# Optimization experiments

Measured on AMD Instinct MI355X. Metric: run time of the kernel, lower is better.

Reference implementation:

```python
import jax, jax.numpy as jnp
import numpy as np

EMBED_DIM = 64
N_EMBED = 1024
BATCH, H, W = 16, 64, 64


def setup_inputs() -> dict:
    key = jax.random.key(0)
    k1, k2 = jax.random.split(key)
    inputs = jax.random.normal(k1, (BATCH, H, W, EMBED_DIM), dtype=jnp.float32)
    # codebook as in Quantize.build: RandomNormal(stddev=1.0), shape (embed_dim, n_embed)
    cluster_mean = jax.random.normal(k2, (EMBED_DIM, N_EMBED), dtype=jnp.float32)
    return {"inputs": inputs, "cluster_mean": cluster_mean}


def reference(inputs, cluster_mean):
    # inputs: [B,H,W,D]; cluster_mean: [D,K]
    D = cluster_mean.shape[0]
    samples = inputs.reshape(-1, D)  # [N,D]
    dist = (
        jnp.sum(samples * samples, axis=1, keepdims=True)
        - 2.0 * (samples @ cluster_mean)
        + jnp.sum(cluster_mean * cluster_mean, axis=0, keepdims=True)
    )
    cluster_index = jnp.argmin(dist, axis=1).reshape(inputs.shape[:-1])  # [B,H,W]
    quantize = cluster_mean.T[cluster_index]  # gather -> [B,H,W,D]
    q_loss = jnp.mean((quantize - jax.lax.stop_gradient(inputs)) ** 2)
    e_loss = jnp.mean((jax.lax.stop_gradient(quantize) - inputs) ** 2)
    loss = q_loss + 0.25 * e_loss
    # straight-through estimator
    outputs = inputs + jax.lax.stop_gradient(quantize - inputs)
    return outputs, cluster_index, loss
```

## Files before the change

### kernel.cpp

```cpp
#include <hip/hip_runtime.h>
#include <stdint.h>

#define NS 65536
#define D 64
#define K 1024
#define NEL 4194304
#define MARGIN 0.05f

typedef short bf16x8 __attribute__((ext_vector_type(8)));
typedef float f32x4 __attribute__((ext_vector_type(4)));

static __device__ __forceinline__ unsigned short bf16_rne(float x) {
    union { float f; uint32_t u; } v; v.f = x;
    uint32_t r = v.u + 0x7FFFu + ((v.u >> 16) & 1u);
    return (unsigned short)(r >> 16);
}
static __device__ __forceinline__ float bf16f(unsigned short h) {
    union { uint32_t u; float f; } v; v.u = ((uint32_t)h) << 16;
    return v.f;
}

__global__ __launch_bounds__(256) void vq_prep(
    const float* __restrict__ cm,
    unsigned short* __restrict__ mhi,
    unsigned short* __restrict__ mlo,
    float* __restrict__ cnorm,
    double* __restrict__ acc)
{
    const int tx = threadIdx.x;
    const int kl = tx & 63, dq = tx >> 6;
    const int k = blockIdx.x * 64 + kl;
    if (blockIdx.x == 0 && tx == 0) *acc = 0.0;

    unsigned short h[16], lo[16];
    float p = 0.f;
#pragma unroll
    for (int j = 0; j < 16; ++j) {
        float v = cm[(dq*16 + j) * K + k];
        unsigned short hb = bf16_rne(v);
        h[j] = hb;
        lo[j] = bf16_rne(v - bf16f(hb));
        p = fmaf(v, v, p);
    }
    bf16x8 v0, v1, w0, w1;
#pragma unroll
    for (int j = 0; j < 8; ++j) {
        v0[j] = (short)h[j];  v1[j] = (short)h[8+j];
        w0[j] = (short)lo[j]; w1[j] = (short)lo[8+j];
    }
    *(bf16x8*)(mhi + (size_t)k*D + dq*16)     = v0;
    *(bf16x8*)(mhi + (size_t)k*D + dq*16 + 8) = v1;
    *(bf16x8*)(mlo + (size_t)k*D + dq*16)     = w0;
    *(bf16x8*)(mlo + (size_t)k*D + dq*16 + 8) = w1;

    __shared__ float pn[4][64];
    pn[dq][kl] = p;
    __syncthreads();
    if (tx < 64)
        cnorm[blockIdx.x*64 + tx] = (pn[0][tx]+pn[1][tx]) + (pn[2][tx]+pn[3][tx]);
}

__global__ __launch_bounds__(256, 4) void vq_main(
    const float* __restrict__ xin,
    const float* __restrict__ cm,
    const unsigned short* __restrict__ mhi,
    const unsigned short* __restrict__ mlo,
    const float* __restrict__ cnorm,
    float* __restrict__ outq,
    float* __restrict__ outidx,
    double* __restrict__ acc_g)
{
    __shared__ char smemA[18432];
    __shared__ unsigned short btile[2][2048];
    __shared__ float cn_lds[1024];
    __shared__ int   widx[64];

    unsigned short* xh = (unsigned short*)smemA;
    unsigned short* xl = (unsigned short*)(smemA + 9216);
    float* mb1 = (float*)smemA;
    float* mb2 = (float*)(smemA + 4096);
    int*   mi1 = (int*)(smemA + 8192);
    int*   mi2 = (int*)(smemA + 12288);
    float* red = (float*)smemA;

    const int tx = threadIdx.x;
    const int S0 = blockIdx.x * 64;
    const int w = tx >> 6, l = tx & 63;
    const int quad = l >> 4, col = l & 15;

    const unsigned short* stage_src = (w & 2) ? mlo : mhi;
    const int qh = ((w & 1) << 2) + quad;
    const unsigned short* stage_gp0 = stage_src + (size_t)col*D + qh*8;

    __builtin_amdgcn_global_load_lds(stage_gp0, &btile[0][w*512], 16, 0, 0);

    {
        const int s = tx >> 2, d0 = (tx & 3) * 16;
        const float* gp = xin + (size_t)(S0 + s) * D + d0;
        bf16x8 hv0, hv1, lv0, lv1;
#pragma unroll
        for (int j = 0; j < 8; ++j) {
            float va = gp[j], vb = gp[8 + j];
            unsigned short ha = bf16_rne(va), hb = bf16_rne(vb);
            hv0[j] = (short)ha; hv1[j] = (short)hb;
            lv0[j] = (short)bf16_rne(va - bf16f(ha));
            lv1[j] = (short)bf16_rne(vb - bf16f(hb));
        }
        *(bf16x8*)(xh + s*72 + d0)     = hv0;
        *(bf16x8*)(xh + s*72 + d0 + 8) = hv1;
        *(bf16x8*)(xl + s*72 + d0)     = lv0;
        *(bf16x8*)(xl + s*72 + d0 + 8) = lv1;
#pragma unroll
        for (int q = 0; q < 4; ++q) cn_lds[q*256 + tx] = cnorm[q*256 + tx];
    }
    __syncthreads();

    const int srow = w*16 + col;
    bf16x8 ahi0 = *(const bf16x8*)(xh + srow*72 + quad*8);
    bf16x8 ahi1 = *(const bf16x8*)(xh + srow*72 + 32 + quad*8);
    bf16x8 alo0 = *(const bf16x8*)(xl + srow*72 + quad*8);
    bf16x8 alo1 = *(const bf16x8*)(xl + srow*72 + 32 + quad*8);

    float b1[4], b2[4]; int i1[4], i2[4];
#pragma unroll
    for (int r = 0; r < 4; ++r) { b1[r]=3.4e38f; b2[r]=3.4e38f; i1[r]=0; i2[r]=0; }

    for (int t = 0; t < 64; ++t) {
        if (t > 0) __syncthreads();
        if (t < 63) {
            const unsigned short* gp = stage_gp0 + (size_t)(t+1)*16*D;
            __builtin_amdgcn_global_load_lds(gp, &btile[(t+1)&1][w*512], 16, 0, 0);
        }
        const unsigned short* bt = btile[t&1];
        bf16x8 bh0 = *(const bf16x8*)(bt + l*8);
        bf16x8 bh1 = *(const bf16x8*)(bt + 512  + l*8);
        bf16x8 bl0 = *(const bf16x8*)(bt + 1024 + l*8);
        bf16x8 bl1 = *(const bf16x8*)(bt + 1536 + l*8);
        f32x4 z = {0.f, 0.f, 0.f, 0.f};
        f32x4 hh = __builtin_amdgcn_mfma_f32_16x16x32_bf16(ahi0, bh0, z, 0,0,0);
        hh       = __builtin_amdgcn_mfma_f32_16x16x32_bf16(ahi1, bh1, hh, 0,0,0);
        f32x4 hl = __builtin_amdgcn_mfma_f32_16x16x32_bf16(ahi0, bl0, z, 0,0,0);
        hl       = __builtin_amdgcn_mfma_f32_16x16x32_bf16(ahi1, bl1, hl, 0,0,0);
        f32x4 lh = __builtin_amdgcn_mfma_f32_16x16x32_bf16(alo0, bh0, z, 0,0,0);
        lh       = __builtin_amdgcn_mfma_f32_16x16x32_bf16(alo1, bh1, lh, 0,0,0);
        const int kcode = t*16 + col;
        const float cn = cn_lds[kcode];
#pragma unroll
        for (int r = 0; r < 4; ++r) {
            float dot = (hh[r] + hl[r]) + lh[r];
            float d = fmaf(-2.f, dot, cn);
            bool c1 = d < b1[r];
            bool c2 = d < b2[r];
            b2[r] = c1 ? b1[r] : (c2 ? d : b2[r]);
            i2[r] = c1 ? i1[r] : (c2 ? kcode : i2[r]);
            b1[r] = c1 ? d : b1[r];
            i1[r] = c1 ? kcode : i1[r];
        }
        __syncthreads();
    }

#pragma unroll
    for (int r = 0; r < 4; ++r) {
        mb1[tx*4 + r] = b1[r];
        mb2[tx*4 + r] = b2[r];
        mi1[tx*4 + r] = i1[r];
        mi2[tx*4 + r] = i2[r];
    }
    __syncthreads();

    if (tx < 64) {
        const int mw = tx >> 4, mq = (tx >> 2) & 3, mr = tx & 3;
        float B1 = 3.4e38f, B2 = 3.4e38f; int I1 = 0, I2 = 0;
#pragma unroll
        for (int c = 0; c < 16; ++c) {
            const int e = (mw*64 + mq*16 + c)*4 + mr;
            float v1 = mb1[e]; int j1 = mi1[e];
            float v2 = mb2[e]; int j2 = mi2[e];
            if (v1 < B1)      { B2 = B1; I2 = I1; B1 = v1; I1 = j1; }
            else if (v1 < B2) { B2 = v1; I2 = j1; }
            if (v2 < B1)      { B2 = B1; I2 = I1; B1 = v2; I1 = j2; }
            else if (v2 < B2) { B2 = v2; I2 = j2; }
        }
        int winner = I1;
        if (B2 - B1 < MARGIN) {
            const float* xp = xin + (size_t)(S0 + tx) * D;
            float a0=0,a1=0,a2=0,a3=0, e0=0,e1=0,e2=0,e3=0;
            for (int dd = 0; dd < D; dd += 4) {
                float x0 = xp[dd], x1 = xp[dd+1], x2 = xp[dd+2], x3 = xp[dd+3];
                a0 = fmaf(x0, cm[(dd+0)*K + I1], a0);
                a1 = fmaf(x1, cm[(dd+1)*K + I1], a1);
                a2 = fmaf(x2, cm[(dd+2)*K + I1], a2);
                a3 = fmaf(x3, cm[(dd+3)*K + I1], a3);
                e0 = fmaf(x0, cm[(dd+0)*K + I2], e0);
                e1 = fmaf(x1, cm[(dd+1)*K + I2], e1);
                e2 = fmaf(x2, cm[(dd+2)*K + I2], e2);
                e3 = fmaf(x3, cm[(dd+3)*K + I2], e3);
            }
            float d1 = fmaf(-2.f, (a0+a1)+(a2+a3), cn_lds[I1]);
            float d2 = fmaf(-2.f, (e0+e1)+(e2+e3), cn_lds[I2]);
            if (d2 < d1 || (d2 == d1 && I2 < I1)) winner = I2;
        }
        widx[tx] = winner;
    }
    __syncthreads();

    const int sl = tx >> 2, d0 = (tx & 3) * 16;
    const int gs = S0 + sl;
    const int wi = widx[sl];
    const unsigned short* mh = mhi + (size_t)wi*D + d0;
    const unsigned short* ml = mlo + (size_t)wi*D + d0;
    bf16x8 h0 = *(const bf16x8*)(mh);
    bf16x8 h1 = *(const bf16x8*)(mh + 8);
    bf16x8 l0 = *(const bf16x8*)(ml);
    bf16x8 l1 = *(const bf16x8*)(ml + 8);
    const float* xr = xin + (size_t)gs*D + d0;
    float* oq = outq + (size_t)gs*D + d0;
    float psum = 0.f;
#pragma unroll
    for (int g = 0; g < 4; ++g) {
        float4 xv = *(const float4*)(xr + 4*g);
        float q0 = bf16f((unsigned short)(g < 2 ? h0[4*g+0] : h1[4*g-8+0])) +
                   bf16f((unsigned short)(g < 2 ? l0[4*g+0] : l1[4*g-8+0]));
        float q1 = bf16f((unsigned short)(g < 2 ? h0[4*g+1] : h1[4*g-8+1])) +
                   bf16f((unsigned short)(g < 2 ? l0[4*g+1] : l1[4*g-8+1]));
        float q2 = bf16f((unsigned short)(g < 2 ? h0[4*g+2] : h1[4*g-8+2])) +
                   bf16f((unsigned short)(g < 2 ? l0[4*g+2] : l1[4*g-8+2]));
        float q3 = bf16f((unsigned short)(g < 2 ? h0[4*g+3] : h1[4*g-8+3])) +
                   bf16f((unsigned short)(g < 2 ? l0[4*g+3] : l1[4*g-8+3]));
        float dx = q0 - xv.x, dy = q1 - xv.y, dz = q2 - xv.z, dw = q3 - xv.w;
        float4 o;
        o.x = xv.x + dx; o.y = xv.y + dy; o.z = xv.z + dz; o.w = xv.w + dw;
        *(float4*)(oq + 4*g) = o;
        psum = fmaf(dx, dx, psum);
        psum = fmaf(dy, dy, psum);
        psum = fmaf(dz, dz, psum);
        psum = fmaf(dw, dw, psum);
    }

    if (tx < 64)
        outidx[S0 + tx] = (float)widx[tx];

    red[tx] = psum;
    __syncthreads();
    for (int st = 128; st > 0; st >>= 1) {
        if (tx < st) red[tx] += red[tx + st];
        __syncthreads();
    }
    if (tx == 0) atomicAdd(acc_g, (double)red[0]);
}

__global__ void vq_finalize(const double* __restrict__ acc,
                            float* __restrict__ loss_out)
{
    float m = (float)(*acc / (double)NEL);
    *loss_out = m + 0.25f * m;
}

extern "C" void kernel_launch(void* const* d_in, const int* in_sizes, int n_in,
                              void* d_out, int out_size, void* d_ws, size_t ws_size,
                              hipStream_t stream) {
    const float* xin = (const float*)d_in[0];
    const float* cm  = (const float*)d_in[1];

    float* out     = (float*)d_out;
    float* outq    = out;
    float* outidx  = out + NEL;
    float* outloss = out + NEL + NS;

    unsigned short* mhi = (unsigned short*)d_ws;
    unsigned short* mlo = mhi + (size_t)K * D;
    float*  cnorm = (float*)((char*)d_ws + 262144);
    double* acc   = (double*)((char*)d_ws + 266240);

    vq_prep<<<16, 256, 0, stream>>>(cm, mhi, mlo, cnorm, acc);
    vq_main<<<1024, 256, 0, stream>>>(xin, cm, mhi, mlo, cnorm, outq, outidx, acc);
    vq_finalize<<<1, 1, 0, stream>>>(acc, outloss);
}
```

Before: 133.6 us.

## Load codebook fragments directly to registers, drop LDS staging and barriers

The main loop no longer stages codebook tiles through LDS with global_load_lds and two barriers per step. Each lane now prefetches its bf16 hi/lo fragments straight from global (L2-resident) into registers one step ahead. The three partial MFMA accumulators are merged into one chain, and the top-2 update uses fmed3/fmin. The prep kernel is spread over more blocks, and the merge scratch is padded to avoid bank conflicts. The aim is to remove barrier stalls and LDS traffic, at the cost of redundant global loads across waves and a serial MFMA dependency chain.

```diff
diff --git a/kernel.cpp b/kernel.cpp
--- a/kernel.cpp
+++ b/kernel.cpp
@@ -8,6 +8,7 @@
 #define MARGIN 0.05f
 
 typedef short bf16x8 __attribute__((ext_vector_type(8)));
+typedef short s16x4 __attribute__((ext_vector_type(4)));
 typedef float f32x4 __attribute__((ext_vector_type(4)));
 
 static __device__ __forceinline__ unsigned short bf16_rne(float x) {
@@ -28,36 +29,33 @@
     double* __restrict__ acc)
 {
     const int tx = threadIdx.x;
-    const int kl = tx & 63, dq = tx >> 6;
-    const int k = blockIdx.x * 64 + kl;
+    const int kl = tx & 15;
+    const int dg = tx >> 4;
+    const int k = blockIdx.x * 16 + kl;
     if (blockIdx.x == 0 && tx == 0) *acc = 0.0;
 
-    unsigned short h[16], lo[16];
     float p = 0.f;
-#pragma unroll
-    for (int j = 0; j < 16; ++j) {
-        float v = cm[(dq*16 + j) * K + k];
+    s16x4 hv, lv;
+#pragma unroll
+    for (int j = 0; j < 4; ++j) {
+        float v = cm[(dg * 4 + j) * K + k];
         unsigned short hb = bf16_rne(v);
-        h[j] = hb;
-        lo[j] = bf16_rne(v - bf16f(hb));
+        hv[j] = (short)hb;
+        lv[j] = (short)bf16_rne(v - bf16f(hb));
         p = fmaf(v, v, p);
     }
-    bf16x8 v0, v1, w0, w1;
-#pragma unroll
-    for (int j = 0; j < 8; ++j) {
-        v0[j] = (short)h[j];  v1[j] = (short)h[8+j];
-        w0[j] = (short)lo[j]; w1[j] = (short)lo[8+j];
-    }
-    *(bf16x8*)(mhi + (size_t)k*D + dq*16)     = v0;
-    *(bf16x8*)(mhi + (size_t)k*D + dq*16 + 8) = v1;
-    *(bf16x8*)(mlo + (size_t)k*D + dq*16)     = w0;
-    *(bf16x8*)(mlo + (size_t)k*D + dq*16 + 8) = w1;
-
-    __shared__ float pn[4][64];
-    pn[dq][kl] = p;
-    __syncthreads();
-    if (tx < 64)
-        cnorm[blockIdx.x*64 + tx] = (pn[0][tx]+pn[1][tx]) + (pn[2][tx]+pn[3][tx]);
+    *(s16x4*)(mhi + (size_t)k * D + dg * 4) = hv;
+    *(s16x4*)(mlo + (size_t)k * D + dg * 4) = lv;
+
+    __shared__ float pn[16][17];
+    pn[kl][dg] = p;
+    __syncthreads();
+    if (tx < 16) {
+        float s = 0.f;
+#pragma unroll
+        for (int g = 0; g < 16; ++g) s += pn[tx][g];
+        cnorm[blockIdx.x * 16 + tx] = s;
+    }
 }
 
 __global__ __launch_bounds__(256, 4) void vq_main(
@@ -71,16 +69,15 @@
     double* __restrict__ acc_g)
 {
     __shared__ char smemA[18432];
-    __shared__ unsigned short btile[2][2048];
     __shared__ float cn_lds[1024];
     __shared__ int   widx[64];
 
     unsigned short* xh = (unsigned short*)smemA;
     unsigned short* xl = (unsigned short*)(smemA + 9216);
     float* mb1 = (float*)smemA;
-    float* mb2 = (float*)(smemA + 4096);
-    int*   mi1 = (int*)(smemA + 8192);
-    int*   mi2 = (int*)(smemA + 12288);
+    float* mb2 = (float*)(smemA + 4352);
+    int*   mi1 = (int*)(smemA + 8704);
+    int*   mi2 = (int*)(smemA + 13056);
     float* red = (float*)smemA;
 
     const int tx = threadIdx.x;
@@ -88,11 +85,12 @@
     const int w = tx >> 6, l = tx & 63;
     const int quad = l >> 4, col = l & 15;
 
-    const unsigned short* stage_src = (w & 2) ? mlo : mhi;
-    const int qh = ((w & 1) << 2) + quad;
-    const unsigned short* stage_gp0 = stage_src + (size_t)col*D + qh*8;
-
-    __builtin_amdgcn_global_load_lds(stage_gp0, &btile[0][w*512], 16, 0, 0);
+    const unsigned short* ph = mhi + (size_t)col * D + quad * 8;
+    const unsigned short* pl = mlo + (size_t)col * D + quad * 8;
+    bf16x8 nh0 = *(const bf16x8*)(ph);
+    bf16x8 nh1 = *(const bf16x8*)(ph + 32);
+    bf16x8 nl0 = *(const bf16x8*)(pl);
+    bf16x8 nl1 = *(const bf16x8*)(pl + 32);
 
     {
         const int s = tx >> 2, d0 = (tx & 3) * 16;
@@ -106,65 +104,63 @@
             lv0[j] = (short)bf16_rne(va - bf16f(ha));
             lv1[j] = (short)bf16_rne(vb - bf16f(hb));
         }
-        *(bf16x8*)(xh + s*72 + d0)     = hv0;
-        *(bf16x8*)(xh + s*72 + d0 + 8) = hv1;
-        *(bf16x8*)(xl + s*72 + d0)     = lv0;
-        *(bf16x8*)(xl + s*72 + d0 + 8) = lv1;
-#pragma unroll
-        for (int q = 0; q < 4; ++q) cn_lds[q*256 + tx] = cnorm[q*256 + tx];
-    }
-    __syncthreads();
-
-    const int srow = w*16 + col;
-    bf16x8 ahi0 = *(const bf16x8*)(xh + srow*72 + quad*8);
-    bf16x8 ahi1 = *(const bf16x8*)(xh + srow*72 + 32 + quad*8);
-    bf16x8 alo0 = *(const bf16x8*)(xl + srow*72 + quad*8);
-    bf16x8 alo1 = *(const bf16x8*)(xl + srow*72 + 32 + quad*8);
+        *(bf16x8*)(xh + s * 72 + d0)     = hv0;
+        *(bf16x8*)(xh + s * 72 + d0 + 8) = hv1;
+        *(bf16x8*)(xl + s * 72 + d0)     = lv0;
+        *(bf16x8*)(xl + s * 72 + d0 + 8) = lv1;
+#pragma unroll
+        for (int q = 0; q < 4; ++q) cn_lds[q * 256 + tx] = cnorm[q * 256 + tx];
+    }
+    __syncthreads();
+
+    const int srow = w * 16 + col;
+    bf16x8 ahi0 = *(const bf16x8*)(xh + srow * 72 + quad * 8);
+    bf16x8 ahi1 = *(const bf16x8*)(xh + srow * 72 + 32 + quad * 8);
+    bf16x8 alo0 = *(const bf16x8*)(xl + srow * 72 + quad * 8);
+    bf16x8 alo1 = *(const bf16x8*)(xl + srow * 72 + 32 + quad * 8);
 
     float b1[4], b2[4]; int i1[4], i2[4];
 #pragma unroll
-    for (int r = 0; r < 4; ++r) { b1[r]=3.4e38f; b2[r]=3.4e38f; i1[r]=0; i2[r]=0; }
-
+    for (int r = 0; r < 4; ++r) { b1[r] = 3.4e38f; b2[r] = 3.4e38f; i1[r] = 0; i2[r] = 0; }
+
+#pragma unroll 2
     for (int t = 0; t < 64; ++t) {
-        if (t > 0) __syncthreads();
+        bf16x8 bh0 = nh0, bh1 = nh1, bl0 = nl0, bl1 = nl1;
+        ph += 16 * D; pl += 16 * D;
         if (t < 63) {
-            const unsigned short* gp = stage_gp0 + (size_t)(t+1)*16*D;
-            __builtin_amdgcn_global_load_lds(gp, &btile[(t+1)&1][w*512], 16, 0, 0);
-        }
-        const unsigned short* bt = btile[t&1];
-        bf16x8 bh0 = *(const bf16x8*)(bt + l*8);
-        bf16x8 bh1 = *(const bf16x8*)(bt + 512  + l*8);
-        bf16x8 bl0 = *(const bf16x8*)(bt + 1024 + l*8);
-        bf16x8 bl1 = *(const bf16x8*)(bt + 1536 + l*8);
-        f32x4 z = {0.f, 0.f, 0.f, 0.f};
-        f32x4 hh = __builtin_amdgcn_mfma_f32_16x16x32_bf16(ahi0, bh0, z, 0,0,0);
-        hh       = __builtin_amdgcn_mfma_f32_16x16x32_bf16(ahi1, bh1, hh, 0,0,0);
-        f32x4 hl = __builtin_amdgcn_mfma_f32_16x16x32_bf16(ahi0, bl0, z, 0,0,0);
-        hl       = __builtin_amdgcn_mfma_f32_16x16x32_bf16(ahi1, bl1, hl, 0,0,0);
-        f32x4 lh = __builtin_amdgcn_mfma_f32_16x16x32_bf16(alo0, bh0, z, 0,0,0);
-        lh       = __builtin_amdgcn_mfma_f32_16x16x32_bf16(alo1, bh1, lh, 0,0,0);
-        const int kcode = t*16 + col;
+            nh0 = *(const bf16x8*)(ph);
+            nh1 = *(const bf16x8*)(ph + 32);
+            nl0 = *(const bf16x8*)(pl);
+            nl1 = *(const bf16x8*)(pl + 32);
+        }
+        const int kcode = t * 16 + col;
         const float cn = cn_lds[kcode];
+        f32x4 acc = {0.f, 0.f, 0.f, 0.f};
+        acc = __builtin_amdgcn_mfma_f32_16x16x32_bf16(ahi0, bh0, acc, 0, 0, 0);
+        acc = __builtin_amdgcn_mfma_f32_16x16x32_bf16(ahi1, bh1, acc, 0, 0, 0);
+        acc = __builtin_amdgcn_mfma_f32_16x16x32_bf16(ahi0, bl0, acc, 0, 0, 0);
+        acc = __builtin_amdgcn_mfma_f32_16x16x32_bf16(ahi1, bl1, acc, 0, 0, 0);
+        acc = __builtin_amdgcn_mfma_f32_16x16x32_bf16(alo0, bh0, acc, 0, 0, 0);
+        acc = __builtin_amdgcn_mfma_f32_16x16x32_bf16(alo1, bh1, acc, 0, 0, 0);
 #pragma unroll
         for (int r = 0; r < 4; ++r) {
-            float dot = (hh[r] + hl[r]) + lh[r];
-            float d = fmaf(-2.f, dot, cn);
-            bool c1 = d < b1[r];
-            bool c2 = d < b2[r];
-            b2[r] = c1 ? b1[r] : (c2 ? d : b2[r]);
+            float dv = fmaf(-2.f, acc[r], cn);
+            bool c1 = dv < b1[r];
+            bool c2 = dv < b2[r];
+            b2[r] = __builtin_amdgcn_fmed3f(b1[r], dv, b2[r]);
+            b1[r] = fminf(b1[r], dv);
             i2[r] = c1 ? i1[r] : (c2 ? kcode : i2[r]);
-            b1[r] = c1 ? d : b1[r];
             i1[r] = c1 ? kcode : i1[r];
         }
-        __syncthreads();
-    }
-
+    }
+
+    const int sk = 4 * (tx + (tx >> 4));
 #pragma unroll
     for (int r = 0; r < 4; ++r) {
-        mb1[tx*4 + r] = b1[r];
-        mb2[tx*4 + r] = b2[r];
-        mi1[tx*4 + r] = i1[r];
-        mi2[tx*4 + r] = i2[r];
+        mb1[sk + r] = b1[r];
+        mb2[sk + r] = b2[r];
+        mi1[sk + r] = i1[r];
+        mi2[sk + r] = i2[r];
     }
     __syncthreads();
 
@@ -173,7 +169,8 @@
         float B1 = 3.4e38f, B2 = 3.4e38f; int I1 = 0, I2 = 0;
 #pragma unroll
         for (int c = 0; c < 16; ++c) {
-            const int e = (mw*64 + mq*16 + c)*4 + mr;
+            const int tw = mw * 64 + mq * 16 + c;
+            const int e = 4 * (tw + (tw >> 4)) + mr;
             float v1 = mb1[e]; int j1 = mi1[e];
             float v2 = mb2[e]; int j2 = mi2[e];
             if (v1 < B1)      { B2 = B1; I2 = I1; B1 = v1; I1 = j1; }
@@ -184,20 +181,20 @@
         int winner = I1;
         if (B2 - B1 < MARGIN) {
             const float* xp = xin + (size_t)(S0 + tx) * D;
-            float a0=0,a1=0,a2=0,a3=0, e0=0,e1=0,e2=0,e3=0;
+            float a0 = 0, a1 = 0, a2 = 0, a3 = 0, e0 = 0, e1 = 0, e2 = 0, e3 = 0;
             for (int dd = 0; dd < D; dd += 4) {
-                float x0 = xp[dd], x1 = xp[dd+1], x2 = xp[dd+2], x3 = xp[dd+3];
-                a0 = fmaf(x0, cm[(dd+0)*K + I1], a0);
-                a1 = fmaf(x1, cm[(dd+1)*K + I1], a1);
-                a2 = fmaf(x2, cm[(dd+2)*K + I1], a2);
-                a3 = fmaf(x3, cm[(dd+3)*K + I1], a3);
-                e0 = fmaf(x0, cm[(dd+0)*K + I2], e0);
-                e1 = fmaf(x1, cm[(dd+1)*K + I2], e1);
-                e2 = fmaf(x2, cm[(dd+2)*K + I2], e2);
-                e3 = fmaf(x3, cm[(dd+3)*K + I2], e3);
+                float x0 = xp[dd], x1 = xp[dd + 1], x2 = xp[dd + 2], x3 = xp[dd + 3];
+                a0 = fmaf(x0, cm[(dd + 0) * K + I1], a0);
+                a1 = fmaf(x1, cm[(dd + 1) * K + I1], a1);
+                a2 = fmaf(x2, cm[(dd + 2) * K + I1], a2);
+                a3 = fmaf(x3, cm[(dd + 3) * K + I1], a3);
+                e0 = fmaf(x0, cm[(dd + 0) * K + I2], e0);
+                e1 = fmaf(x1, cm[(dd + 1) * K + I2], e1);
+                e2 = fmaf(x2, cm[(dd + 2) * K + I2], e2);
+                e3 = fmaf(x3, cm[(dd + 3) * K + I2], e3);
             }
-            float d1 = fmaf(-2.f, (a0+a1)+(a2+a3), cn_lds[I1]);
-            float d2 = fmaf(-2.f, (e0+e1)+(e2+e3), cn_lds[I2]);
+            float d1 = fmaf(-2.f, (a0 + a1) + (a2 + a3), cn_lds[I1]);
+            float d2 = fmaf(-2.f, (e0 + e1) + (e2 + e3), cn_lds[I2]);
             if (d2 < d1 || (d2 == d1 && I2 < I1)) winner = I2;
         }
         widx[tx] = winner;
@@ -207,30 +204,30 @@
     const int sl = tx >> 2, d0 = (tx & 3) * 16;
     const int gs = S0 + sl;
     const int wi = widx[sl];
-    const unsigned short* mh = mhi + (size_t)wi*D + d0;
-    const unsigned short* ml = mlo + (size_t)wi*D + d0;
+    const unsigned short* mh = mhi + (size_t)wi * D + d0;
+    const unsigned short* ml = mlo + (size_t)wi * D + d0;
     bf16x8 h0 = *(const bf16x8*)(mh);
     bf16x8 h1 = *(const bf16x8*)(mh + 8);
     bf16x8 l0 = *(const bf16x8*)(ml);
     bf16x8 l1 = *(const bf16x8*)(ml + 8);
-    const float* xr = xin + (size_t)gs*D + d0;
-    float* oq = outq + (size_t)gs*D + d0;
+    const float* xr = xin + (size_t)gs * D + d0;
+    float* oq = outq + (size_t)gs * D + d0;
     float psum = 0.f;
 #pragma unroll
     for (int g = 0; g < 4; ++g) {
-        float4 xv = *(const float4*)(xr + 4*g);
-        float q0 = bf16f((unsigned short)(g < 2 ? h0[4*g+0] : h1[4*g-8+0])) +
-                   bf16f((unsigned short)(g < 2 ? l0[4*g+0] : l1[4*g-8+0]));
-        float q1 = bf16f((unsigned short)(g < 2 ? h0[4*g+1] : h1[4*g-8+1])) +
-                   bf16f((unsigned short)(g < 2 ? l0[4*g+1] : l1[4*g-8+1]));
-        float q2 = bf16f((unsigned short)(g < 2 ? h0[4*g+2] : h1[4*g-8+2])) +
-                   bf16f((unsigned short)(g < 2 ? l0[4*g+2] : l1[4*g-8+2]));
-        float q3 = bf16f((unsigned short)(g < 2 ? h0[4*g+3] : h1[4*g-8+3])) +
-                   bf16f((unsigned short)(g < 2 ? l0[4*g+3] : l1[4*g-8+3]));
+        float4 xv = *(const float4*)(xr + 4 * g);
+        float q0 = bf16f((unsigned short)(g < 2 ? h0[4 * g + 0] : h1[4 * g - 8 + 0])) +
+                   bf16f((unsigned short)(g < 2 ? l0[4 * g + 0] : l1[4 * g - 8 + 0]));
+        float q1 = bf16f((unsigned short)(g < 2 ? h0[4 * g + 1] : h1[4 * g - 8 + 1])) +
+                   bf16f((unsigned short)(g < 2 ? l0[4 * g + 1] : l1[4 * g - 8 + 1]));
+        float q2 = bf16f((unsigned short)(g < 2 ? h0[4 * g + 2] : h1[4 * g - 8 + 2])) +
+                   bf16f((unsigned short)(g < 2 ? l0[4 * g + 2] : l1[4 * g - 8 + 2]));
+        float q3 = bf16f((unsigned short)(g < 2 ? h0[4 * g + 3] : h1[4 * g - 8 + 3])) +
+                   bf16f((unsigned short)(g < 2 ? l0[4 * g + 3] : l1[4 * g - 8 + 3]));
         float dx = q0 - xv.x, dy = q1 - xv.y, dz = q2 - xv.z, dw = q3 - xv.w;
         float4 o;
         o.x = xv.x + dx; o.y = xv.y + dy; o.z = xv.z + dz; o.w = xv.w + dw;
-        *(float4*)(oq + 4*g) = o;
+        *(float4*)(oq + 4 * g) = o;
         psum = fmaf(dx, dx, psum);
         psum = fmaf(dy, dy, psum);
         psum = fmaf(dz, dz, psum);
@@ -272,7 +269,7 @@
     float*  cnorm = (float*)((char*)d_ws + 262144);
     double* acc   = (double*)((char*)d_ws + 266240);
 
-    vq_prep<<<16, 256, 0, stream>>>(cm, mhi, mlo, cnorm, acc);
+    vq_prep<<<64, 256, 0, stream>>>(cm, mhi, mlo, cnorm, acc);
     vq_main<<<1024, 256, 0, stream>>>(xin, cm, mhi, mlo, cnorm, outq, outidx, acc);
     vq_finalize<<<1, 1, 0, stream>>>(acc, outloss);
 }
```

Measured after the change: 197.6 us. 47.8% more time.
